# Optimization experiments

Hardware: AMD Instinct MI355X
Metric: run time of the kernel (lower is better)

Reference implementation:

```python
import jax, jax.numpy as jnp
import numpy as np

B, G, L, S = 4096, 16000, 64, 20000  # batch spots, genes, labels, total spots
LOG_2PI = float(np.log(2.0 * np.pi))


def _log_nb_positive_altparam(x, r, o):
    # NB with total_count r > 0 and logits o (stereoscope parametrization)
    return (jax.lax.lgamma(x + r) - jax.lax.lgamma(r) - jax.lax.lgamma(x + 1.0)
            + x * jax.nn.log_sigmoid(o) + r * jax.nn.log_sigmoid(-o))


def setup_inputs() -> dict:
    key = jax.random.key(0)
    ks = jax.random.split(key, 8)
    x = jax.random.randint(ks[0], (B, G), 0, 100, dtype=jnp.int32)
    y = jax.random.randint(ks[1], (B, 1), 0, L, dtype=jnp.int32)
    ind_x = jax.random.randint(ks[2], (B, 1), 0, S, dtype=jnp.int32)
    W = jax.random.normal(ks[3], (G, L), dtype=jnp.float32)          # fixed dictionary
    px_o = 0.5 * jax.random.normal(ks[4], (G,), dtype=jnp.float32)   # fixed log-odds
    eta = jax.random.normal(ks[5], (G,), dtype=jnp.float32)
    V = jax.random.normal(ks[6], (L + 1, S), dtype=jnp.float32)
    beta = 0.1 * jax.random.normal(ks[7], (G,), dtype=jnp.float32)
    return {"x": x, "y": y, "ind_x": ind_x, "W": W, "px_o": px_o,
            "eta": eta, "V": V, "beta": beta}


def reference(x, y, ind_x, W, px_o, eta, V, beta):
    x_f = x.astype(jnp.float32)                      # [B, G]
    beta_sp = jax.nn.softplus(beta)                  # [G]
    w_sp = jax.nn.softplus(W)                        # [G, L]
    eps_sp = jax.nn.softplus(eta)                    # [G]
    # r_hat = [beta*W | eps]  -> [G, L+1]
    r_hat = jnp.concatenate([beta_sp[:, None] * w_sp, eps_sp[:, None]], axis=1)
    # column-gather from V (embedding lookup over spots), then softplus
    v_ind = jax.nn.softplus(V[:, ind_x[:, 0]])       # [L+1, B]
    # thin matmul, inner dim L+1; px_rate: [B, G]
    px_rate = jnp.einsum("gl,lb->bg", r_hat, v_ind)
    # NB reconstruction loss per spot
    reconst_loss = -jnp.sum(_log_nb_positive_altparam(x_f, px_rate, px_o[None, :]), axis=-1)  # [B]
    # -sum log N(eta; 0, 1)
    neg_log_likelihood_prior = jnp.sum(0.5 * LOG_2PI + 0.5 * eta * eta)
    return (reconst_loss, jnp.float32(0.0), neg_log_likelihood_prior)
```

## Files before the change

### kernel.cpp

```cpp
#include <hip/hip_runtime.h>
#include <hip/hip_bf16.h>
#include <math.h>

#define Gn 16000
#define Bn 4096
#define Ln 64
#define Sn 20000

typedef __attribute__((ext_vector_type(8))) short bf16x8;
typedef __attribute__((ext_vector_type(4))) float f32x4;


__device__ __forceinline__ float softplus_precise(float z) {
    return fmaxf(z, 0.0f) + log1pf(__expf(-fabsf(z)));
}

__device__ __forceinline__ float lgamma_pos8(float z) {
    float p = z * (z + 1.f) * (z + 2.f) * (z + 3.f)
                * (z + 4.f) * (z + 5.f) * (z + 6.f) * (z + 7.f);
    float w = z + 8.f;
    return (w - 0.5f) * __logf(w) - w + 0.9189385332046727f
           + __fdividef(1.0f, 12.0f * w) - __logf(p);
}

__device__ __forceinline__ unsigned short f2bf(float f) {
    union { float f; unsigned int u; } v; v.f = f;
    unsigned int r = v.u + 0x7fff + ((v.u >> 16) & 1);
    return (unsigned short)(r >> 16);
}


__global__ void prep_genes(const float* __restrict__ W,
                           const float* __restrict__ px_o,
                           const float* __restrict__ eta,
                           const float* __restrict__ beta,
                           unsigned short* __restrict__ rhB,
                           float* __restrict__ lsp1,
                           float* __restrict__ lsn,
                           float* __restrict__ eps) {
    int idx = blockIdx.x * 256 + threadIdx.x;
    int g = idx >> 6;
    float bsp = softplus_precise(beta[g]);
    rhB[idx] = f2bf(bsp * softplus_precise(W[idx]));
    if (idx < Gn) {
        eps[idx] = softplus_precise(eta[idx]);
        float o = px_o[idx];
        lsp1[idx] = -softplus_precise(-o) - 1.0f;
        lsn[idx]  = -softplus_precise(o);
    }
}

__global__ void prep_spots(const float* __restrict__ V,
                           const int* __restrict__ ind_x,
                           unsigned short* __restrict__ vBg,
                           float* __restrict__ v64) {
    int idx = blockIdx.x * 256 + threadIdx.x;
    int b = idx >> 6, l = idx & 63;
    int s = ind_x[b];
    vBg[idx] = f2bf(softplus_precise(V[l * Sn + s]));
    if (idx < Bn) {
        int s2 = ind_x[idx];
        v64[idx] = softplus_precise(V[Ln * Sn + s2]);
    }
}

__global__ void prior_kernel(const float* __restrict__ eta, float* __restrict__ out) {
    int idx = blockIdx.x * 256 + threadIdx.x;
    float s = 0.f;
    if (idx < Gn) {
        float e = eta[idx];
        s = 0.9189385332046727f + 0.5f * e * e;
    }
    #pragma unroll
    for (int off = 32; off; off >>= 1) s += __shfl_xor(s, off, 64);
    __shared__ float red[4];
    if ((threadIdx.x & 63) == 0) red[threadIdx.x >> 6] = s;
    __syncthreads();
    if (threadIdx.x == 0) atomicAdd(&out[Bn + 1], red[0] + red[1] + red[2] + red[3]);
}


__global__ __launch_bounds__(256, 4) void main_kernel(
    const int*            __restrict__ x,
    const unsigned short* __restrict__ rhB,
    const unsigned short* __restrict__ vBg,
    const float*          __restrict__ v64,
    const float*          __restrict__ lsp1g,
    const float*          __restrict__ lsng,
    const float*          __restrict__ epsg,
    float*                __restrict__ out) {
    __shared__ float lfact[100];

    const int tid = threadIdx.x;
    if (tid < 100) lfact[tid] = lgamma_pos8((float)tid + 1.0f);
    __syncthreads();

    const int g0 = blockIdx.x * 64;
    const int b0 = blockIdx.y * 64;
    const int wave = tid >> 6, lane = tid & 63;
    const int quad = lane >> 4, ln = lane & 15;
    const int mrow  = wave * 16 + ln;
    const int brow0 = b0 + wave * 16 + quad * 4;

    const unsigned short* aPtr = vBg + (size_t)(b0 + mrow) * 64 + quad * 8;
    bf16x8 af0 = *(const bf16x8*)(aPtr);
    bf16x8 af1 = *(const bf16x8*)(aPtr + 32);

    const unsigned short* bPtr = rhB + (size_t)(g0 + ln) * 64 + quad * 8;
    bf16x8 bf_[4][2];
    #pragma unroll
    for (int nb = 0; nb < 4; nb++) {
        bf_[nb][0] = *(const bf16x8*)(bPtr + nb * 1024);
        bf_[nb][1] = *(const bf16x8*)(bPtr + nb * 1024 + 32);
    }

    int xv[4][4];
    #pragma unroll
    for (int r = 0; r < 4; r++) {
        const int* xp = x + (size_t)(brow0 + r) * Gn + g0 + ln;
        #pragma unroll
        for (int nb = 0; nb < 4; nb++) xv[nb][r] = xp[nb * 16];
    }

    float vvr[4];
    #pragma unroll
    for (int r = 0; r < 4; r++) vvr[r] = v64[brow0 + r];
    float lsp1v[4], lsnv[4], ev4[4];
    #pragma unroll
    for (int nb = 0; nb < 4; nb++) {
        int g = g0 + nb * 16 + ln;
        lsp1v[nb] = lsp1g[g];
        lsnv[nb]  = lsng[g];
        ev4[nb]   = epsg[g];
    }

    f32x4 acc[4];
    #pragma unroll
    for (int nb = 0; nb < 4; nb++) acc[nb] = (f32x4){0.f, 0.f, 0.f, 0.f};
    #pragma unroll
    for (int nb = 0; nb < 4; nb++) {
        acc[nb] = __builtin_amdgcn_mfma_f32_16x16x32_bf16(af0, bf_[nb][0], acc[nb], 0, 0, 0);
        acc[nb] = __builtin_amdgcn_mfma_f32_16x16x32_bf16(af1, bf_[nb][1], acc[nb], 0, 0, 0);
    }

    float rowpart[4] = {0.f, 0.f, 0.f, 0.f};
    #pragma unroll
    for (int nb = 0; nb < 4; nb++) {
        #pragma unroll
        for (int r = 0; r < 4; r++) {
            const float rr = fmaf(ev4[nb], vvr[r], acc[nb][r]);
            const int   xi = xv[nb][r];
            const float xf = (float)xi;
            const float s  = rr + xf;
            float t = fmaf(s - 0.5f, __logf(s), -lfact[xi]);
            t = fmaf(-(rr - 0.5f), __logf(rr), t);
            t = fmaf(xf, lsp1v[nb], t);
            t = fmaf(rr, lsnv[nb], t);
            rowpart[r] += t;
        }
    }

    #pragma unroll
    for (int r = 0; r < 4; r++) {
        float v = rowpart[r];
        v += __shfl_xor(v, 1, 64);
        v += __shfl_xor(v, 2, 64);
        v += __shfl_xor(v, 4, 64);
        v += __shfl_xor(v, 8, 64);
        if (ln == 0) atomicAdd(&out[brow0 + r], -v);
    }
}


extern "C" void kernel_launch(void* const* d_in, const int* in_sizes, int n_in,
                              void* d_out, int out_size, void* d_ws, size_t ws_size,
                              hipStream_t stream) {
    const int*   x     = (const int*)d_in[0];
    const int*   ind_x = (const int*)d_in[2];
    const float* W     = (const float*)d_in[3];
    const float* px_o  = (const float*)d_in[4];
    const float* eta   = (const float*)d_in[5];
    const float* V     = (const float*)d_in[6];
    const float* beta  = (const float*)d_in[7];
    float* out = (float*)d_out;

    char* wsb = (char*)d_ws;
    unsigned short* rhB  = (unsigned short*)(wsb);
    unsigned short* vBg  = (unsigned short*)(wsb + 2048000);
    float*          v64  = (float*)(wsb + 2572288);
    float*          lsp1 = (float*)(wsb + 2588672);
    float*          lsn  = (float*)(wsb + 2652672);
    float*          eps  = (float*)(wsb + 2716672);

    hipMemsetAsync(d_out, 0, (Bn + 2) * sizeof(float), stream);

    prep_genes<<<(Gn * 64) / 256, 256, 0, stream>>>(W, px_o, eta, beta, rhB, lsp1, lsn, eps);
    prep_spots<<<(Bn * 64) / 256, 256, 0, stream>>>(V, ind_x, vBg, v64);
    prior_kernel<<<(Gn + 255) / 256, 256, 0, stream>>>(eta, out);

    dim3 grid(Gn / 64, Bn / 64);
    main_kernel<<<grid, 256, 0, stream>>>(x, rhB, vBg, v64, lsp1, lsn, eps, out);
}
```

Before: 445.1 us.

## Permute gene columns so each lane loads contiguous int4 x and float4 params

The prep kernel now writes the bf16 gene dictionary with a permuted gene order inside each 64-gene block. As a result, MFMA output column nb of lane ln corresponds to gene g0+ln*4+nb. This lets each lane load its x counts and per-gene parameters as 16-byte vectors instead of strided scalar loads, cutting load instruction count. The loads are issued before the MFMAs, and the occupancy hint in launch bounds is dropped, which may change register allocation.

```diff
diff --git a/kernel.cpp b/kernel.cpp
--- a/kernel.cpp
+++ b/kernel.cpp
@@ -39,9 +39,11 @@
                            float* __restrict__ lsn,
                            float* __restrict__ eps) {
     int idx = blockIdx.x * 256 + threadIdx.x;
-    int g = idx >> 6;
+    int g = idx >> 6, l = idx & 63;
+    int j = g & 63, gb = g & ~63;
+    int c = (j & 3) * 16 + (j >> 2);
     float bsp = softplus_precise(beta[g]);
-    rhB[idx] = f2bf(bsp * softplus_precise(W[idx]));
+    rhB[(size_t)(gb + c) * 64 + l] = f2bf(bsp * softplus_precise(W[idx]));
     if (idx < Gn) {
         eps[idx] = softplus_precise(eta[idx]);
         float o = px_o[idx];
@@ -80,7 +82,7 @@
 }
 
 
-__global__ __launch_bounds__(256, 4) void main_kernel(
+__global__ __launch_bounds__(256) void main_kernel(
     const int*            __restrict__ x,
     const unsigned short* __restrict__ rhB,
     const unsigned short* __restrict__ vBg,
@@ -102,6 +104,16 @@
     const int mrow  = wave * 16 + ln;
     const int brow0 = b0 + wave * 16 + quad * 4;
 
+    int4 xq[4];
+    #pragma unroll
+    for (int r = 0; r < 4; r++)
+        xq[r] = *(const int4*)(x + (size_t)(brow0 + r) * Gn + g0 + ln * 4);
+
+    const float4 lsp1q = *(const float4*)(lsp1g + g0 + ln * 4);
+    const float4 lsnq  = *(const float4*)(lsng  + g0 + ln * 4);
+    const float4 epsq  = *(const float4*)(epsg  + g0 + ln * 4);
+    const float4 vq    = *(const float4*)(v64 + brow0);
+
     const unsigned short* aPtr = vBg + (size_t)(b0 + mrow) * 64 + quad * 8;
     bf16x8 af0 = *(const bf16x8*)(aPtr);
     bf16x8 af1 = *(const bf16x8*)(aPtr + 32);
@@ -114,26 +126,6 @@
         bf_[nb][1] = *(const bf16x8*)(bPtr + nb * 1024 + 32);
     }
 
-    int xv[4][4];
-    #pragma unroll
-    for (int r = 0; r < 4; r++) {
-        const int* xp = x + (size_t)(brow0 + r) * Gn + g0 + ln;
-        #pragma unroll
-        for (int nb = 0; nb < 4; nb++) xv[nb][r] = xp[nb * 16];
-    }
-
-    float vvr[4];
-    #pragma unroll
-    for (int r = 0; r < 4; r++) vvr[r] = v64[brow0 + r];
-    float lsp1v[4], lsnv[4], ev4[4];
-    #pragma unroll
-    for (int nb = 0; nb < 4; nb++) {
-        int g = g0 + nb * 16 + ln;
-        lsp1v[nb] = lsp1g[g];
-        lsnv[nb]  = lsng[g];
-        ev4[nb]   = epsg[g];
-    }
-
     f32x4 acc[4];
     #pragma unroll
     for (int nb = 0; nb < 4; nb++) acc[nb] = (f32x4){0.f, 0.f, 0.f, 0.f};
@@ -142,6 +134,11 @@
         acc[nb] = __builtin_amdgcn_mfma_f32_16x16x32_bf16(af0, bf_[nb][0], acc[nb], 0, 0, 0);
         acc[nb] = __builtin_amdgcn_mfma_f32_16x16x32_bf16(af1, bf_[nb][1], acc[nb], 0, 0, 0);
     }
+
+    const float vvr[4]  = {vq.x, vq.y, vq.z, vq.w};
+    const float lsp1v[4] = {lsp1q.x, lsp1q.y, lsp1q.z, lsp1q.w};
+    const float lsnv[4]  = {lsnq.x, lsnq.y, lsnq.z, lsnq.w};
+    const float ev4[4]   = {epsq.x, epsq.y, epsq.z, epsq.w};
 
     float rowpart[4] = {0.f, 0.f, 0.f, 0.f};
     #pragma unroll
@@ -149,7 +146,7 @@
         #pragma unroll
         for (int r = 0; r < 4; r++) {
             const float rr = fmaf(ev4[nb], vvr[r], acc[nb][r]);
-            const int   xi = xv[nb][r];
+            const int   xi = ((const int*)&xq[r])[nb];
             const float xf = (float)xi;
             const float s  = rr + xf;
             float t = fmaf(s - 0.5f, __logf(s), -lfact[xi]);
```

Measured after the change: 442.4 us. About the same (-0.6%).
